# Performance work log

Measured on AMD Instinct MI355X. Metric: run time of the kernel, lower is better.

Reference implementation:

```python
import jax, jax.numpy as jnp
import numpy as np


def setup_inputs() -> dict:
    key = jax.random.key(0)
    k = jax.random.split(key, 5)
    bs, n_heads, ch, n_obj, emb = 4, 8, 64, 8, 64
    ih = iw = 32
    T = ih * iw
    return {
        "qkv": jax.random.normal(k[0], (bs, 3 * n_heads * ch, T), dtype=jnp.float32),
        "bboxes": jax.random.uniform(k[1], (bs, n_obj, 5), dtype=jnp.float32),
        "null_prompt_emb": jax.random.normal(k[2], (bs, emb, T), dtype=jnp.float32),
        "prompt_emb": jax.random.normal(k[3], (bs, emb, T), dtype=jnp.float32),
        "W_prompt": jax.random.normal(k[4], (3 * n_heads * ch, emb), dtype=jnp.float32) * 0.02,
        "n_heads": n_heads,
        "image_h": ih,
        "image_w": iw,
    }


def _region_masks(bboxes, h, w):
    # Faithful translation of get_region: bbox unpacked as (x, y, width, height, obj_idx).
    # Returns float masks [b, n_obj, h*w].
    x, y, bw, bh = bboxes[..., 0], bboxes[..., 1], bboxes[..., 2], bboxes[..., 3]
    i0 = jnp.minimum(float(h) - 1.0, jnp.floor(y * h))
    j0 = jnp.minimum(float(w) - 1.0, jnp.floor(x * w))
    i1 = i0 + jnp.maximum(1.0, jnp.ceil(bh * h))
    j1 = j0 + jnp.maximum(1.0, jnp.ceil(bw * w))
    ii = jnp.arange(h, dtype=jnp.float32)
    jj = jnp.arange(w, dtype=jnp.float32)
    mi = (ii >= i0[..., None]) & (ii < i1[..., None])          # [b, n, h]
    mj = (jj >= j0[..., None]) & (jj < j1[..., None])          # [b, n, w]
    m = (mi[..., :, None] & mj[..., None, :]).astype(jnp.float32)  # [b, n, h, w]
    return m.reshape(m.shape[0], m.shape[1], h * w)


def reference(qkv, bboxes, null_prompt_emb, prompt_emb, W_prompt, n_heads, image_h, image_w):
    bs, width, T = qkv.shape
    ch = width // (3 * n_heads)
    scale = float(ch) ** -0.25  # 1/sqrt(sqrt(ch))

    def split3(x):
        x = x.reshape(bs * n_heads, 3 * ch, T)
        return x[:, :ch], x[:, ch:2 * ch], x[:, 2 * ch:]

    q, k, v = split3(qkv)
    # to_prompt_token is a 1x1 Conv1d (no bias) == matmul over the channel dim
    nq, nk, nv = split3(jnp.einsum('oc,bct->bot', W_prompt, null_prompt_emb))
    pq, pk, pv = split3(jnp.einsum('oc,bct->bot', W_prompt, prompt_emb))

    def attn(qh, kh, vh, col_mask=None):
        w = jnp.einsum('bct,bcs->bts', qh * scale, kh * scale)
        if col_mask is not None:
            w = jnp.where(col_mask[:, None, :] > 0.5, w, -1e9)
        w = jax.nn.softmax(w.astype(jnp.float32), axis=-1).astype(qh.dtype)
        return jnp.einsum('bts,bcs->btc', w, vh)  # [bs*heads, T, ch]

    # global (null-prompt) attention
    a_null = attn(q + nq, k + nk, v + nv)

    # per-object masked attention, blended by region masks
    masks = _region_masks(bboxes, image_h, image_w)       # [bs, n_obj, T]
    masks = jnp.repeat(masks, n_heads, axis=0)            # [(bs*heads), n_obj, T]
    qf, kf, vf = q + pq, k + pk, v + pv
    a_fg = jnp.zeros_like(a_null)
    counter = jnp.zeros((bs * n_heads, T, 1), dtype=jnp.float32)
    for o in range(masks.shape[1]):  # small fixed loop over objects
        m = masks[:, o]                                   # [bs*heads, T]
        a_fg = a_fg + m[:, :, None] * attn(qf, kf, vf, col_mask=m)
        counter = counter + m[:, :, None]
    fg = counter > 0.5
    a_final = jnp.where(fg, a_fg, a_null) / jnp.where(fg, counter, 1.0)
    return jnp.transpose(a_final, (0, 2, 1)).reshape(bs, n_heads * ch, T)
```

## Files before the change

### kernel.cpp

```cpp
#include <hip/hip_runtime.h>
#include <math.h>

#define BS 4
#define NH 8
#define TT 1024
#define WROWS 1536
#define NOBJ 8
#define NT 65536

#define QNT_OFF  0
#define KNT_OFF  2097152
#define VNCS_OFF 4194304
#define QFT_OFF  6291456
#define KFT_OFF  8388608
#define VFT_OFF  10485760

typedef __attribute__((ext_vector_type(8))) short short8;
typedef __attribute__((ext_vector_type(4))) float v4f;

__device__ __forceinline__ short f2bf(float f) {
    unsigned u = __float_as_uint(f);
    u = (u + 0x7FFF + ((u >> 16) & 1)) >> 16;
    return (short)u;
}
__device__ __forceinline__ unsigned p2(float a, float b) {
    return (unsigned)(unsigned short)f2bf(a) | ((unsigned)(unsigned short)f2bf(b) << 16);
}
__device__ __forceinline__ unsigned p2t(float a, float b) {
    return (__float_as_uint(a) >> 16) | (__float_as_uint(b) & 0xFFFF0000u);
}

__device__ __forceinline__ void get_region(const float* __restrict__ bb,
                                           int& i0, int& j0, int& hh, int& ww) {
    float x = bb[0], y = bb[1], bw = bb[2], bh = bb[3];
    float i0f = fminf(31.0f, floorf(y * 32.0f));
    float j0f = fminf(31.0f, floorf(x * 32.0f));
    float i1f = i0f + fmaxf(1.0f, ceilf(bh * 32.0f));
    float j1f = j0f + fmaxf(1.0f, ceilf(bw * 32.0f));
    i0 = (int)i0f; j0 = (int)j0f;
    int i1 = min(32, (int)i1f);
    int j1 = min(32, (int)j1f);
    hh = i1 - i0; ww = j1 - j0;
}

__global__ __launch_bounds__(256)
void fuse_kernel(const float* __restrict__ qkv, const float* __restrict__ nEmb,
                 const float* __restrict__ pEmb, const float* __restrict__ W,
                 short* __restrict__ wsS) {
    __shared__ float WtT[64][68];
    __shared__ float En[64][64];
    __shared__ float Ep[64][64];
    short* sbuf = (short*)&WtT[0][0];
    int t0 = blockIdx.x * 64;
    int r0 = blockIdx.y * 64;
    int b  = blockIdx.z;
    int tid = threadIdx.x;
    int half = tid >> 4;
    int q4 = (tid & 15) * 4;
#pragma unroll
    for (int p = 0; p < 4; ++p) {
        int rr = p * 16 + half;
        float4 w4 = *(const float4*)&W[(r0 + rr) * 64 + q4];
        WtT[q4 + 0][rr] = w4.x; WtT[q4 + 1][rr] = w4.y;
        WtT[q4 + 2][rr] = w4.z; WtT[q4 + 3][rr] = w4.w;
        int e = p * 16 + half;
        *(float4*)&En[e][q4] = *(const float4*)&nEmb[(b * 64 + e) * TT + t0 + q4];
        *(float4*)&Ep[e][q4] = *(const float4*)&pEmb[(b * 64 + e) * TT + t0 + q4];
    }
    __syncthreads();
    int tr = tid >> 4, tc = tid & 15;
    float an[4][4] = {{0.f}}, ap[4][4] = {{0.f}};
#pragma unroll 8
    for (int e = 0; e < 64; ++e) {
        float4 w4 = *(const float4*)&WtT[e][tr * 4];
        float4 n4 = *(const float4*)&En[e][tc * 4];
        float4 p4 = *(const float4*)&Ep[e][tc * 4];
        float w[4]  = {w4.x, w4.y, w4.z, w4.w};
        float nn[4] = {n4.x, n4.y, n4.z, n4.w};
        float pp[4] = {p4.x, p4.y, p4.z, p4.w};
#pragma unroll
        for (int i = 0; i < 4; ++i)
#pragma unroll
            for (int j = 0; j < 4; ++j) {
                an[i][j] += w[i] * nn[j];
                ap[i][j] += w[i] * pp[j];
            }
    }
    int sec = (r0 % 192) / 64;
    int h = r0 / 192, bh = b * 8 + h;
    float sc = (sec == 0) ? 0.125f : 1.0f;
#pragma unroll
    for (int i = 0; i < 4; ++i) {
        int r = r0 + tr * 4 + i;
        float4 x4 = *(const float4*)&qkv[(b * WROWS + r) * TT + t0 + tc * 4];
        an[i][0] = (an[i][0] + x4.x) * sc; an[i][1] = (an[i][1] + x4.y) * sc;
        an[i][2] = (an[i][2] + x4.z) * sc; an[i][3] = (an[i][3] + x4.w) * sc;
        ap[i][0] = (ap[i][0] + x4.x) * sc; ap[i][1] = (ap[i][1] + x4.y) * sc;
        ap[i][2] = (ap[i][2] + x4.z) * sc; ap[i][3] = (ap[i][3] + x4.w) * sc;
    }
    if (sec == 2) {
        short* Vn = wsS + VNCS_OFF + bh * NT;
#pragma unroll
        for (int i = 0; i < 4; ++i) {
            int c = tr * 4 + i;
            uint2 pk; pk.x = p2(an[i][0], an[i][1]); pk.y = p2(an[i][2], an[i][3]);
            *(uint2*)&Vn[c * TT + t0 + tc * 4] = pk;
        }
        short* dst = wsS + VFT_OFF + bh * NT + t0 * 64;
        __syncthreads();
#pragma unroll
        for (int i = 0; i < 4; ++i)
#pragma unroll
            for (int j = 0; j < 4; ++j)
                sbuf[(tc * 4 + j) * 72 + tr * 4 + i] = f2bf(ap[i][j]);
        __syncthreads();
#pragma unroll
        for (int rep = 0; rep < 2; ++rep) {
            int idx = rep * 256 + tid; int tl = idx >> 3, c8 = idx & 7;
            *(short8*)&dst[tl * 64 + c8 * 8] = *(const short8*)&sbuf[tl * 72 + c8 * 8];
        }
    } else {
        short* dn = wsS + (sec == 0 ? QNT_OFF : KNT_OFF) + bh * NT + t0 * 64;
        short* df = wsS + (sec == 0 ? QFT_OFF : KFT_OFF) + bh * NT + t0 * 64;
        __syncthreads();
#pragma unroll
        for (int i = 0; i < 4; ++i)
#pragma unroll
            for (int j = 0; j < 4; ++j)
                sbuf[(tc * 4 + j) * 72 + tr * 4 + i] = f2bf(an[i][j]);
        __syncthreads();
#pragma unroll
        for (int rep = 0; rep < 2; ++rep) {
            int idx = rep * 256 + tid; int tl = idx >> 3, c8 = idx & 7;
            *(short8*)&dn[tl * 64 + c8 * 8] = *(const short8*)&sbuf[tl * 72 + c8 * 8];
        }
        __syncthreads();
#pragma unroll
        for (int i = 0; i < 4; ++i)
#pragma unroll
            for (int j = 0; j < 4; ++j)
                sbuf[(tc * 4 + j) * 72 + tr * 4 + i] = f2bf(ap[i][j]);
        __syncthreads();
#pragma unroll
        for (int rep = 0; rep < 2; ++rep) {
            int idx = rep * 256 + tid; int tl = idx >> 3, c8 = idx & 7;
            *(short8*)&df[tl * 64 + c8 * 8] = *(const short8*)&sbuf[tl * 72 + c8 * 8];
        }
    }
}

__global__ __launch_bounds__(128)
void attn_fused(const short* __restrict__ wsS, const float* __restrict__ bboxes,
                float* __restrict__ out) {
    __shared__ __align__(16) short lds[11520];
    __shared__ unsigned short tmap[1024];
    short* Qs = lds;
    short* Ks = lds + 2304;
    short* Vs = lds + 6912;
    int bh = blockIdx.x, rt = blockIdx.y;
    int b = bh >> 3, h = bh & 7;
    int t0 = rt * 32;
    int tid = threadIdx.x;
    int w = tid >> 6, lane = tid & 63, ln = lane & 15, qd = lane >> 4;
    const short* QnT = wsS + QNT_OFF + bh * NT;
    const short* KnT = wsS + KNT_OFF + bh * NT;
    const short* Vn  = wsS + VNCS_OFF + bh * NT;
    const short* QfT = wsS + QFT_OFF + bh * NT;
    const short* KfT = wsS + KFT_OFF + bh * NT;
    const short* VfT = wsS + VFT_OFF + bh * NT;

    unsigned inter = 0u, cover = 0u;
    for (int o = 0; o < NOBJ; ++o) {
        int i0, j0, hh, ww;
        get_region(&bboxes[(b * NOBJ + o) * 5], i0, j0, hh, ww);
        if (i0 <= rt && rt < i0 + hh) {
            inter |= (1u << o);
            unsigned wm = (ww >= 32) ? 0xFFFFFFFFu : (((1u << ww) - 1u) << j0);
            cover |= wm;
        }
    }

    v4f Onull[4];
#pragma unroll
    for (int cc = 0; cc < 4; ++cc) Onull[cc] = (v4f){0.f, 0.f, 0.f, 0.f};

    if (cover != 0xFFFFFFFFu) {
#pragma unroll
        for (int rep = 0; rep < 2; ++rep) {
            int idx = rep * 128 + tid; int cell = idx >> 3, o8 = idx & 7;
            *(short8*)&Qs[cell * 72 + o8 * 8] =
                *(const short8*)&QnT[(t0 + cell) * 64 + o8 * 8];
        }
        __syncthreads();
        short8 aq0 = *(const short8*)&Qs[(16 * w + ln) * 72 + qd * 8];
        short8 aq1 = *(const short8*)&Qs[(16 * w + ln) * 72 + 32 + qd * 8];
        v4f O[4]; float l[4];
#pragma unroll
        for (int r = 0; r < 4; ++r) l[r] = 0.f;
#pragma unroll
        for (int cc = 0; cc < 4; ++cc) O[cc] = (v4f){0.f, 0.f, 0.f, 0.f};
        short8 kreg[4], vreg[4];
#pragma unroll
        for (int rep = 0; rep < 4; ++rep) {
            int idx = rep * 128 + tid; int cell = idx >> 3, o8 = idx & 7;
            int pc = 4 * (cell & 15) + (cell >> 4);
            kreg[rep] = *(const short8*)&KnT[pc * 64 + o8 * 8];
            vreg[rep] = *(const short8*)&Vn[cell * TT + o8 * 8];
        }
        for (int ct = 0; ct < 16; ++ct) {
            __syncthreads();
#pragma unroll
            for (int rep = 0; rep < 4; ++rep) {
                int idx = rep * 128 + tid; int cell = idx >> 3, o8 = idx & 7;
                *(short8*)&Ks[cell * 72 + o8 * 8] = kreg[rep];
                *(short8*)&Vs[cell * 72 + o8 * 8] = vreg[rep];
            }
            __syncthreads();
            if (ct < 15) {
                int s0 = (ct + 1) * 64;
#pragma unroll
                for (int rep = 0; rep < 4; ++rep) {
                    int idx = rep * 128 + tid; int cell = idx >> 3, o8 = idx & 7;
                    int pc = 4 * (cell & 15) + (cell >> 4);
                    kreg[rep] = *(const short8*)&KnT[(s0 + pc) * 64 + o8 * 8];
                    vreg[rep] = *(const short8*)&Vn[cell * TT + s0 + o8 * 8];
                }
            }
            v4f S[4];
#pragma unroll
            for (int nn = 0; nn < 4; ++nn) {
                short8 b0 = *(const short8*)&Ks[(nn * 16 + ln) * 72 + qd * 8];
                short8 b1 = *(const short8*)&Ks[(nn * 16 + ln) * 72 + 32 + qd * 8];
                v4f z = (v4f){0.f, 0.f, 0.f, 0.f};
                z = __builtin_amdgcn_mfma_f32_16x16x32_bf16(aq0, b0, z, 0, 0, 0);
                z = __builtin_amdgcn_mfma_f32_16x16x32_bf16(aq1, b1, z, 0, 0, 0);
                S[nn] = z;
            }
#pragma unroll
            for (int r = 0; r < 4; ++r) {
                float e0 = __expf(S[0][r]);
                float e1 = __expf(S[1][r]);
                float e2 = __expf(S[2][r]);
                float e3 = __expf(S[3][r]);
                l[r] += e0 + e1 + e2 + e3;
                uint2 pk; pk.x = p2t(e0, e1); pk.y = p2t(e2, e3);
                *(uint2*)&Qs[(w * 16 + 4 * qd + r) * 72 + 4 * ln] = pk;
            }
            short8 ap0 = *(const short8*)&Qs[(w * 16 + ln) * 72 + qd * 8];
            short8 ap1 = *(const short8*)&Qs[(w * 16 + ln) * 72 + 32 + qd * 8];
#pragma unroll
            for (int cc = 0; cc < 4; ++cc) {
                short8 bv0 = *(const short8*)&Vs[(cc * 16 + ln) * 72 + qd * 8];
                short8 bv1 = *(const short8*)&Vs[(cc * 16 + ln) * 72 + 32 + qd * 8];
                O[cc] = __builtin_amdgcn_mfma_f32_16x16x32_bf16(ap0, bv0, O[cc], 0, 0, 0);
                O[cc] = __builtin_amdgcn_mfma_f32_16x16x32_bf16(ap1, bv1, O[cc], 0, 0, 0);
            }
        }
#pragma unroll
        for (int r = 0; r < 4; ++r) {
            float rs = l[r];
            rs += __shfl_xor(rs, 1, 64);
            rs += __shfl_xor(rs, 2, 64);
            rs += __shfl_xor(rs, 4, 64);
            rs += __shfl_xor(rs, 8, 64);
            float inv = 1.0f / rs;
#pragma unroll
            for (int cc = 0; cc < 4; ++cc) Onull[cc][r] = O[cc][r] * inv;
        }
    }

    v4f Oacc[4]; float cnt[4];
#pragma unroll
    for (int r = 0; r < 4; ++r) cnt[r] = 0.f;
#pragma unroll
    for (int cc = 0; cc < 4; ++cc) Oacc[cc] = (v4f){0.f, 0.f, 0.f, 0.f};

    if (inter != 0u) {
        __syncthreads();
#pragma unroll
        for (int rep = 0; rep < 2; ++rep) {
            int idx = rep * 128 + tid; int cell = idx >> 3, o8 = idx & 7;
            *(short8*)&Qs[cell * 72 + o8 * 8] =
                *(const short8*)&QfT[(t0 + cell) * 64 + o8 * 8];
        }
        __syncthreads();
        short8 aq0 = *(const short8*)&Qs[(16 * w + ln) * 72 + qd * 8];
        short8 aq1 = *(const short8*)&Qs[(16 * w + ln) * 72 + 32 + qd * 8];
        for (int o = 0; o < NOBJ; ++o) {
            if (!((inter >> o) & 1u)) continue;
            int i0, j0, hh, ww;
            get_region(&bboxes[(b * NOBJ + o) * 5], i0, j0, hh, ww);
            int R = hh * ww;
            for (int idx = tid; idx < R; idx += 128) {
                int ri = idx / ww; int rj = idx - ri * ww;
                tmap[idx] = (unsigned short)((i0 + ri) * 32 + j0 + rj);
            }
            __syncthreads();
            v4f O[4]; float l[4];
#pragma unroll
            for (int r = 0; r < 4; ++r) l[r] = 0.f;
#pragma unroll
            for (int cc = 0; cc < 4; ++cc) O[cc] = (v4f){0.f, 0.f, 0.f, 0.f};
            int nct = (R + 63) >> 6;
            short8 kreg[4], vreg[4];
#pragma unroll
            for (int rep = 0; rep < 4; ++rep) {
                int idx = rep * 128 + tid; int cell = idx >> 3, o8 = idx & 7;
                int pc = 4 * (cell & 15) + (cell >> 4);
                int tk = tmap[min(pc, R - 1)];
                int tv = tmap[min(cell, R - 1)];
                kreg[rep] = *(const short8*)&KfT[tk * 64 + o8 * 8];
                vreg[rep] = *(const short8*)&VfT[tv * 64 + o8 * 8];
            }
            for (int ct = 0; ct < nct; ++ct) {
                int sb = ct * 64;
                __syncthreads();
#pragma unroll
                for (int rep = 0; rep < 4; ++rep) {
                    int idx = rep * 128 + tid; int cell = idx >> 3, o8 = idx & 7;
                    *(short8*)&Ks[cell * 72 + o8 * 8] = kreg[rep];
#pragma unroll
                    for (int jj = 0; jj < 8; ++jj) {
                        int j = (jj + o8) & 7;
                        Vs[(o8 * 8 + j) * 72 + cell] = vreg[rep][j];
                    }
                }
                __syncthreads();
                if (ct + 1 < nct) {
                    int s0 = sb + 64;
#pragma unroll
                    for (int rep = 0; rep < 4; ++rep) {
                        int idx = rep * 128 + tid; int cell = idx >> 3, o8 = idx & 7;
                        int pc = 4 * (cell & 15) + (cell >> 4);
                        int tk = tmap[min(s0 + pc, R - 1)];
                        int tv = tmap[min(s0 + cell, R - 1)];
                        kreg[rep] = *(const short8*)&KfT[tk * 64 + o8 * 8];
                        vreg[rep] = *(const short8*)&VfT[tv * 64 + o8 * 8];
                    }
                }
                v4f S[4];
#pragma unroll
                for (int nn = 0; nn < 4; ++nn) {
                    short8 b0 = *(const short8*)&Ks[(nn * 16 + ln) * 72 + qd * 8];
                    short8 b1 = *(const short8*)&Ks[(nn * 16 + ln) * 72 + 32 + qd * 8];
                    v4f z = (v4f){0.f, 0.f, 0.f, 0.f};
                    z = __builtin_amdgcn_mfma_f32_16x16x32_bf16(aq0, b0, z, 0, 0, 0);
                    z = __builtin_amdgcn_mfma_f32_16x16x32_bf16(aq1, b1, z, 0, 0, 0);
                    S[nn] = z;
                }
                float v0 = (sb + 4 * ln + 0) < R ? 1.f : 0.f;
                float v1 = (sb + 4 * ln + 1) < R ? 1.f : 0.f;
                float v2 = (sb + 4 * ln + 2) < R ? 1.f : 0.f;
                float v3 = (sb + 4 * ln + 3) < R ? 1.f : 0.f;
#pragma unroll
                for (int r = 0; r < 4; ++r) {
                    float e0 = __expf(S[0][r]) * v0;
                    float e1 = __expf(S[1][r]) * v1;
                    float e2 = __expf(S[2][r]) * v2;
                    float e3 = __expf(S[3][r]) * v3;
                    l[r] += e0 + e1 + e2 + e3;
                    uint2 pk; pk.x = p2t(e0, e1); pk.y = p2t(e2, e3);
                    *(uint2*)&Qs[(w * 16 + 4 * qd + r) * 72 + 4 * ln] = pk;
                }
                short8 ap0 = *(const short8*)&Qs[(w * 16 + ln) * 72 + qd * 8];
                short8 ap1 = *(const short8*)&Qs[(w * 16 + ln) * 72 + 32 + qd * 8];
#pragma unroll
                for (int cc = 0; cc < 4; ++cc) {
                    short8 bv0 = *(const short8*)&Vs[(cc * 16 + ln) * 72 + qd * 8];
                    short8 bv1 = *(const short8*)&Vs[(cc * 16 + ln) * 72 + 32 + qd * 8];
                    O[cc] = __builtin_amdgcn_mfma_f32_16x16x32_bf16(ap0, bv0, O[cc], 0, 0, 0);
                    O[cc] = __builtin_amdgcn_mfma_f32_16x16x32_bf16(ap1, bv1, O[cc], 0, 0, 0);
                }
            }
#pragma unroll
            for (int r = 0; r < 4; ++r) {
                float rs = l[r];
                rs += __shfl_xor(rs, 1, 64);
                rs += __shfl_xor(rs, 2, 64);
                rs += __shfl_xor(rs, 4, 64);
                rs += __shfl_xor(rs, 8, 64);
                float inv = 1.0f / rs;
                int tj = 16 * w + 4 * qd + r;
                bool in = (tj >= j0) && (tj < j0 + ww);
                if (in) {
                    cnt[r] += 1.f;
#pragma unroll
                    for (int cc = 0; cc < 4; ++cc) Oacc[cc][r] += O[cc][r] * inv;
                }
            }
        }
    }

    __syncthreads();
    float* Ot = (float*)(lds + 2304);
#pragma unroll
    for (int r = 0; r < 4; ++r) {
        int tl = 16 * w + 4 * qd + r;
        float icnt = cnt[r] > 0.f ? 1.0f / cnt[r] : 0.f;
#pragma unroll
        for (int cc = 0; cc < 4; ++cc) {
            float val = cnt[r] > 0.f ? Oacc[cc][r] * icnt : Onull[cc][r];
            Ot[(cc * 16 + ln) * 36 + tl] = val;
        }
    }
    __syncthreads();
    int obase = (b * 512 + h * 64) * TT + t0;
#pragma unroll
    for (int rep = 0; rep < 4; ++rep) {
        int idx = rep * 128 + tid; int c = idx >> 3, t4 = (idx & 7) * 4;
        *(float4*)&out[obase + c * TT + t4] = *(float4*)&Ot[c * 36 + t4];
    }
}

extern "C" void kernel_launch(void* const* d_in, const int* in_sizes, int n_in,
                              void* d_out, int out_size, void* d_ws, size_t ws_size,
                              hipStream_t stream) {
    const float* qkv    = (const float*)d_in[0];
    const float* bboxes = (const float*)d_in[1];
    const float* nEmb   = (const float*)d_in[2];
    const float* pEmb   = (const float*)d_in[3];
    const float* W      = (const float*)d_in[4];
    short* wsS = (short*)d_ws;
    float* out = (float*)d_out;

    fuse_kernel<<<dim3(16, 24, 4), 256, 0, stream>>>(qkv, nEmb, pEmb, W, wsS);
    attn_fused<<<dim3(32, 32), 128, 0, stream>>>(wsS, bboxes, out);
}
```

Measured before the change: 170.1 us.

## Process two image rows per attention block and switch softmax to exp2

Measured after the change: 162.1 us. 1.05x faster.

```diff
diff --git a/kernel.cpp b/kernel.cpp
--- a/kernel.cpp
+++ b/kernel.cpp
@@ -17,6 +17,12 @@
 
 typedef __attribute__((ext_vector_type(8))) short short8;
 typedef __attribute__((ext_vector_type(4))) float v4f;
+
+#if __has_builtin(__builtin_amdgcn_exp2f)
+#define EXP2(x) __builtin_amdgcn_exp2f(x)
+#else
+#define EXP2(x) exp2f(x)
+#endif
 
 __device__ __forceinline__ short f2bf(float f) {
     unsigned u = __float_as_uint(f);
@@ -50,13 +56,19 @@
     __shared__ float WtT[64][68];
     __shared__ float En[64][64];
     __shared__ float Ep[64][64];
-    short* sbuf = (short*)&WtT[0][0];
+    short* sbufA = (short*)&WtT[0][0];
+    short* sbufB = (short*)&En[0][0];
     int t0 = blockIdx.x * 64;
     int r0 = blockIdx.y * 64;
     int b  = blockIdx.z;
     int tid = threadIdx.x;
     int half = tid >> 4;
     int q4 = (tid & 15) * 4;
+    int tr = tid >> 4, tc = tid & 15;
+    float4 xq[4];
+#pragma unroll
+    for (int i = 0; i < 4; ++i)
+        xq[i] = *(const float4*)&qkv[(b * WROWS + r0 + tr * 4 + i) * TT + t0 + tc * 4];
 #pragma unroll
     for (int p = 0; p < 4; ++p) {
         int rr = p * 16 + half;
@@ -68,7 +80,6 @@
         *(float4*)&Ep[e][q4] = *(const float4*)&pEmb[(b * 64 + e) * TT + t0 + q4];
     }
     __syncthreads();
-    int tr = tid >> 4, tc = tid & 15;
     float an[4][4] = {{0.f}}, ap[4][4] = {{0.f}};
 #pragma unroll 8
     for (int e = 0; e < 64; ++e) {
@@ -88,11 +99,10 @@
     }
     int sec = (r0 % 192) / 64;
     int h = r0 / 192, bh = b * 8 + h;
-    float sc = (sec == 0) ? 0.125f : 1.0f;
+    float sc = (sec == 0) ? 0.18033688f : 1.0f;
 #pragma unroll
     for (int i = 0; i < 4; ++i) {
-        int r = r0 + tr * 4 + i;
-        float4 x4 = *(const float4*)&qkv[(b * WROWS + r) * TT + t0 + tc * 4];
+        float4 x4 = xq[i];
         an[i][0] = (an[i][0] + x4.x) * sc; an[i][1] = (an[i][1] + x4.y) * sc;
         an[i][2] = (an[i][2] + x4.z) * sc; an[i][3] = (an[i][3] + x4.w) * sc;
         ap[i][0] = (ap[i][0] + x4.x) * sc; ap[i][1] = (ap[i][1] + x4.y) * sc;
@@ -112,12 +122,12 @@
         for (int i = 0; i < 4; ++i)
 #pragma unroll
             for (int j = 0; j < 4; ++j)
-                sbuf[(tc * 4 + j) * 72 + tr * 4 + i] = f2bf(ap[i][j]);
+                sbufB[(tc * 4 + j) * 72 + tr * 4 + i] = f2bf(ap[i][j]);
         __syncthreads();
 #pragma unroll
         for (int rep = 0; rep < 2; ++rep) {
             int idx = rep * 256 + tid; int tl = idx >> 3, c8 = idx & 7;
-            *(short8*)&dst[tl * 64 + c8 * 8] = *(const short8*)&sbuf[tl * 72 + c8 * 8];
+            *(short8*)&dst[tl * 64 + c8 * 8] = *(const short8*)&sbufB[tl * 72 + c8 * 8];
         }
     } else {
         short* dn = wsS + (sec == 0 ? QNT_OFF : KNT_OFF) + bh * NT + t0 * 64;
@@ -126,40 +136,31 @@
 #pragma unroll
         for (int i = 0; i < 4; ++i)
 #pragma unroll
-            for (int j = 0; j < 4; ++j)
-                sbuf[(tc * 4 + j) * 72 + tr * 4 + i] = f2bf(an[i][j]);
+            for (int j = 0; j < 4; ++j) {
+                sbufA[(tc * 4 + j) * 72 + tr * 4 + i] = f2bf(an[i][j]);
+                sbufB[(tc * 4 + j) * 72 + tr * 4 + i] = f2bf(ap[i][j]);
+            }
         __syncthreads();
 #pragma unroll
         for (int rep = 0; rep < 2; ++rep) {
             int idx = rep * 256 + tid; int tl = idx >> 3, c8 = idx & 7;
-            *(short8*)&dn[tl * 64 + c8 * 8] = *(const short8*)&sbuf[tl * 72 + c8 * 8];
-        }
-        __syncthreads();
-#pragma unroll
-        for (int i = 0; i < 4; ++i)
-#pragma unroll
-            for (int j = 0; j < 4; ++j)
-                sbuf[(tc * 4 + j) * 72 + tr * 4 + i] = f2bf(ap[i][j]);
-        __syncthreads();
-#pragma unroll
-        for (int rep = 0; rep < 2; ++rep) {
-            int idx = rep * 256 + tid; int tl = idx >> 3, c8 = idx & 7;
-            *(short8*)&df[tl * 64 + c8 * 8] = *(const short8*)&sbuf[tl * 72 + c8 * 8];
-        }
-    }
-}
-
-__global__ __launch_bounds__(128)
+            *(short8*)&dn[tl * 64 + c8 * 8] = *(const short8*)&sbufA[tl * 72 + c8 * 8];
+            *(short8*)&df[tl * 64 + c8 * 8] = *(const short8*)&sbufB[tl * 72 + c8 * 8];
+        }
+    }
+}
+
+__global__ __launch_bounds__(256)
 void attn_fused(const short* __restrict__ wsS, const float* __restrict__ bboxes,
                 float* __restrict__ out) {
-    __shared__ __align__(16) short lds[11520];
+    __shared__ __align__(16) short lds[13824];
     __shared__ unsigned short tmap[1024];
     short* Qs = lds;
-    short* Ks = lds + 2304;
-    short* Vs = lds + 6912;
+    short* Ks = lds + 4608;
+    short* Vs = lds + 9216;
     int bh = blockIdx.x, rt = blockIdx.y;
     int b = bh >> 3, h = bh & 7;
-    int t0 = rt * 32;
+    int t0 = rt * 64;
     int tid = threadIdx.x;
     int w = tid >> 6, lane = tid & 63, ln = lane & 15, qd = lane >> 4;
     const short* QnT = wsS + QNT_OFF + bh * NT;
@@ -169,14 +170,17 @@
     const short* KfT = wsS + KFT_OFF + bh * NT;
     const short* VfT = wsS + VFT_OFF + bh * NT;
 
-    unsigned inter = 0u, cover = 0u;
+    int r0i = 2 * rt, r1i = 2 * rt + 1;
+    unsigned inter = 0u, cov0 = 0u, cov1 = 0u;
     for (int o = 0; o < NOBJ; ++o) {
         int i0, j0, hh, ww;
         get_region(&bboxes[(b * NOBJ + o) * 5], i0, j0, hh, ww);
-        if (i0 <= rt && rt < i0 + hh) {
+        int i1 = i0 + hh;
+        if (i0 <= r1i && i1 > r0i) {
             inter |= (1u << o);
             unsigned wm = (ww >= 32) ? 0xFFFFFFFFu : (((1u << ww) - 1u) << j0);
-            cover |= wm;
+            if (i0 <= r0i && r0i < i1) cov0 |= wm;
+            if (i0 <= r1i && r1i < i1) cov1 |= wm;
         }
     }
 
@@ -184,10 +188,10 @@
 #pragma unroll
     for (int cc = 0; cc < 4; ++cc) Onull[cc] = (v4f){0.f, 0.f, 0.f, 0.f};
 
-    if (cover != 0xFFFFFFFFu) {
+    if ((cov0 & cov1) != 0xFFFFFFFFu) {
 #pragma unroll
         for (int rep = 0; rep < 2; ++rep) {
-            int idx = rep * 128 + tid; int cell = idx >> 3, o8 = idx & 7;
+            int idx = rep * 256 + tid; int cell = idx >> 3, o8 = idx & 7;
             *(short8*)&Qs[cell * 72 + o8 * 8] =
                 *(const short8*)&QnT[(t0 + cell) * 64 + o8 * 8];
         }
@@ -199,10 +203,10 @@
         for (int r = 0; r < 4; ++r) l[r] = 0.f;
 #pragma unroll
         for (int cc = 0; cc < 4; ++cc) O[cc] = (v4f){0.f, 0.f, 0.f, 0.f};
-        short8 kreg[4], vreg[4];
-#pragma unroll
-        for (int rep = 0; rep < 4; ++rep) {
-            int idx = rep * 128 + tid; int cell = idx >> 3, o8 = idx & 7;
+        short8 kreg[2], vreg[2];
+#pragma unroll
+        for (int rep = 0; rep < 2; ++rep) {
+            int idx = rep * 256 + tid; int cell = idx >> 3, o8 = idx & 7;
             int pc = 4 * (cell & 15) + (cell >> 4);
             kreg[rep] = *(const short8*)&KnT[pc * 64 + o8 * 8];
             vreg[rep] = *(const short8*)&Vn[cell * TT + o8 * 8];
@@ -210,8 +214,8 @@
         for (int ct = 0; ct < 16; ++ct) {
             __syncthreads();
 #pragma unroll
-            for (int rep = 0; rep < 4; ++rep) {
-                int idx = rep * 128 + tid; int cell = idx >> 3, o8 = idx & 7;
+            for (int rep = 0; rep < 2; ++rep) {
+                int idx = rep * 256 + tid; int cell = idx >> 3, o8 = idx & 7;
                 *(short8*)&Ks[cell * 72 + o8 * 8] = kreg[rep];
                 *(short8*)&Vs[cell * 72 + o8 * 8] = vreg[rep];
             }
@@ -219,8 +223,8 @@
             if (ct < 15) {
                 int s0 = (ct + 1) * 64;
 #pragma unroll
-                for (int rep = 0; rep < 4; ++rep) {
-                    int idx = rep * 128 + tid; int cell = idx >> 3, o8 = idx & 7;
+                for (int rep = 0; rep < 2; ++rep) {
+                    int idx = rep * 256 + tid; int cell = idx >> 3, o8 = idx & 7;
                     int pc = 4 * (cell & 15) + (cell >> 4);
                     kreg[rep] = *(const short8*)&KnT[(s0 + pc) * 64 + o8 * 8];
                     vreg[rep] = *(const short8*)&Vn[cell * TT + s0 + o8 * 8];
@@ -238,10 +242,10 @@
             }
 #pragma unroll
             for (int r = 0; r < 4; ++r) {
-                float e0 = __expf(S[0][r]);
-                float e1 = __expf(S[1][r]);
-                float e2 = __expf(S[2][r]);
-                float e3 = __expf(S[3][r]);
+                float e0 = EXP2(S[0][r]);
+                float e1 = EXP2(S[1][r]);
+                float e2 = EXP2(S[2][r]);
+                float e3 = EXP2(S[3][r]);
                 l[r] += e0 + e1 + e2 + e3;
                 uint2 pk; pk.x = p2t(e0, e1); pk.y = p2t(e2, e3);
                 *(uint2*)&Qs[(w * 16 + 4 * qd + r) * 72 + 4 * ln] = pk;
@@ -279,7 +283,7 @@
         __syncthreads();
 #pragma unroll
         for (int rep = 0; rep < 2; ++rep) {
-            int idx = rep * 128 + tid; int cell = idx >> 3, o8 = idx & 7;
+            int idx = rep * 256 + tid; int cell = idx >> 3, o8 = idx & 7;
             *(short8*)&Qs[cell * 72 + o8 * 8] =
                 *(const short8*)&QfT[(t0 + cell) * 64 + o8 * 8];
         }
@@ -290,8 +294,9 @@
             if (!((inter >> o) & 1u)) continue;
             int i0, j0, hh, ww;
             get_region(&bboxes[(b * NOBJ + o) * 5], i0, j0, hh, ww);
+            int i1 = i0 + hh;
             int R = hh * ww;
-            for (int idx = tid; idx < R; idx += 128) {
+            for (int idx = tid; idx < R; idx += 256) {
                 int ri = idx / ww; int rj = idx - ri * ww;
                 tmap[idx] = (unsigned short)((i0 + ri) * 32 + j0 + rj);
             }
@@ -302,10 +307,10 @@
 #pragma unroll
             for (int cc = 0; cc < 4; ++cc) O[cc] = (v4f){0.f, 0.f, 0.f, 0.f};
             int nct = (R + 63) >> 6;
-            short8 kreg[4], vreg[4];
-#pragma unroll
-            for (int rep = 0; rep < 4; ++rep) {
-                int idx = rep * 128 + tid; int cell = idx >> 3, o8 = idx & 7;
+            short8 kreg[2], vreg[2];
+#pragma unroll
+            for (int rep = 0; rep < 2; ++rep) {
+                int idx = rep * 256 + tid; int cell = idx >> 3, o8 = idx & 7;
                 int pc = 4 * (cell & 15) + (cell >> 4);
                 int tk = tmap[min(pc, R - 1)];
                 int tv = tmap[min(cell, R - 1)];
@@ -316,8 +321,8 @@
                 int sb = ct * 64;
                 __syncthreads();
 #pragma unroll
-                for (int rep = 0; rep < 4; ++rep) {
-                    int idx = rep * 128 + tid; int cell = idx >> 3, o8 = idx & 7;
+                for (int rep = 0; rep < 2; ++rep) {
+                    int idx = rep * 256 + tid; int cell = idx >> 3, o8 = idx & 7;
                     *(short8*)&Ks[cell * 72 + o8 * 8] = kreg[rep];
 #pragma unroll
                     for (int jj = 0; jj < 8; ++jj) {
@@ -329,8 +334,8 @@
                 if (ct + 1 < nct) {
                     int s0 = sb + 64;
 #pragma unroll
-                    for (int rep = 0; rep < 4; ++rep) {
-                        int idx = rep * 128 + tid; int cell = idx >> 3, o8 = idx & 7;
+                    for (int rep = 0; rep < 2; ++rep) {
+                        int idx = rep * 256 + tid; int cell = idx >> 3, o8 = idx & 7;
                         int pc = 4 * (cell & 15) + (cell >> 4);
                         int tk = tmap[min(s0 + pc, R - 1)];
                         int tv = tmap[min(s0 + cell, R - 1)];
@@ -354,10 +359,10 @@
                 float v3 = (sb + 4 * ln + 3) < R ? 1.f : 0.f;
 #pragma unroll
                 for (int r = 0; r < 4; ++r) {
-                    float e0 = __expf(S[0][r]) * v0;
-                    float e1 = __expf(S[1][r]) * v1;
-                    float e2 = __expf(S[2][r]) * v2;
-                    float e3 = __expf(S[3][r]) * v3;
+                    float e0 = EXP2(S[0][r]) * v0;
+                    float e1 = EXP2(S[1][r]) * v1;
+                    float e2 = EXP2(S[2][r]) * v2;
+                    float e3 = EXP2(S[3][r]) * v3;
                     l[r] += e0 + e1 + e2 + e3;
                     uint2 pk; pk.x = p2t(e0, e1); pk.y = p2t(e2, e3);
                     *(uint2*)&Qs[(w * 16 + 4 * qd + r) * 72 + 4 * ln] = pk;
@@ -380,8 +385,9 @@
                 rs += __shfl_xor(rs, 4, 64);
                 rs += __shfl_xor(rs, 8, 64);
                 float inv = 1.0f / rs;
-                int tj = 16 * w + 4 * qd + r;
-                bool in = (tj >= j0) && (tj < j0 + ww);
+                int t = t0 + 16 * w + 4 * qd + r;
+                int ti = t >> 5, tj = t & 31;
+                bool in = (ti >= i0) && (ti < i1) && (tj >= j0) && (tj < j0 + ww);
                 if (in) {
                     cnt[r] += 1.f;
 #pragma unroll
@@ -392,7 +398,7 @@
     }
 
     __syncthreads();
-    float* Ot = (float*)(lds + 2304);
+    float* Ot = (float*)lds;
 #pragma unroll
     for (int r = 0; r < 4; ++r) {
         int tl = 16 * w + 4 * qd + r;
@@ -400,15 +406,15 @@
 #pragma unroll
         for (int cc = 0; cc < 4; ++cc) {
             float val = cnt[r] > 0.f ? Oacc[cc][r] * icnt : Onull[cc][r];
-            Ot[(cc * 16 + ln) * 36 + tl] = val;
+            Ot[(cc * 16 + ln) * 68 + tl] = val;
         }
     }
     __syncthreads();
     int obase = (b * 512 + h * 64) * TT + t0;
 #pragma unroll
     for (int rep = 0; rep < 4; ++rep) {
-        int idx = rep * 128 + tid; int c = idx >> 3, t4 = (idx & 7) * 4;
-        *(float4*)&out[obase + c * TT + t4] = *(float4*)&Ot[c * 36 + t4];
+        int idx = rep * 256 + tid; int c = idx >> 4, t4 = (idx & 15) * 4;
+        *(float4*)&out[obase + c * TT + t4] = *(float4*)&Ot[c * 68 + t4];
     }
 }
 
@@ -424,5 +430,5 @@
     float* out = (float*)d_out;
 
     fuse_kernel<<<dim3(16, 24, 4), 256, 0, stream>>>(qkv, nEmb, pEmb, W, wsS);
-    attn_fused<<<dim3(32, 32), 128, 0, stream>>>(wsS, bboxes, out);
-}
+    attn_fused<<<dim3(32, 16), 256, 0, stream>>>(wsS, bboxes, out);
+}
```
